# Optimization experiments

Hardware: AMD Instinct MI355X
Metric: run time of the kernel (lower is better)

## Reference

```python
import jax, jax.numpy as jnp
import numpy as np

B, C, T, H, W = 2, 512, 4, 32, 32
NH = 8          # num_heads
GROUPS = 32     # GroupNorm groups
EPS = 1e-5      # GroupNorm eps (torch default)


def setup_inputs() -> dict:
    key = jax.random.key(0)
    k0, k1, k2 = jax.random.split(key, 3)
    s = 0.02
    return {
        "x": jax.random.normal(k0, (B, C, T, H, W), jnp.float32),
        "gn_w": jnp.ones((C,), jnp.float32),
        "gn_b": jnp.zeros((C,), jnp.float32),
        "qkv_w": jax.random.normal(k1, (3 * C, C), jnp.float32) * s,
        "qkv_b": jnp.zeros((3 * C,), jnp.float32),
        "out_w": jax.random.normal(k2, (C, C), jnp.float32) * s,
        "out_b": jnp.zeros((C,), jnp.float32),
    }


def reference(x, gn_w, gn_b, qkv_w, qkv_b, out_w, out_b):
    Bb, Cc, Tt, Hh, Ww = x.shape
    N = Tt * Hh * Ww
    hd = Cc // NH

    # GroupNorm(32, C): normalize over (C//G, T, H, W) per group, biased var
    xg = x.reshape(Bb, GROUPS, -1)
    mean = jnp.mean(xg, axis=-1, keepdims=True)
    var = jnp.var(xg, axis=-1, keepdims=True)
    h = ((xg - mean) * jax.lax.rsqrt(var + EPS)).reshape(Bb, Cc, N)
    h = h * gn_w[None, :, None] + gn_b[None, :, None]

    # 1x1 Conv3d qkv == per-token linear over channels
    qkv = jnp.einsum('oc,bcn->bon', qkv_w, h) + qkv_b[None, :, None]
    qkv = qkv.reshape(Bb, 3, NH, hd, N).transpose(1, 0, 2, 4, 3)  # [3,B,nh,N,hd]
    q, k, v = qkv[0], qkv[1], qkv[2]

    scale = 1.0 / np.sqrt(hd).astype(np.float32)
    attn = jax.nn.softmax(jnp.einsum('bhnd,bhmd->bhnm', q, k) * scale, axis=-1)
    o = jnp.einsum('bhnm,bhmd->bhnd', attn, v)  # [B,nh,N,hd]

    # Faithful to original: h.permute(1,2,0,3).reshape(B,C,T,H,W)
    o = o.transpose(1, 2, 0, 3).reshape(Bb, Cc, N)
    o = jnp.einsum('oc,bcn->bon', out_w, o) + out_b[None, :, None]
    return x + o.reshape(Bb, Cc, Tt, Hh, Ww)
```

## Files before the change

### kernel.cpp

```cpp
#include <hip/hip_runtime.h>
#include <stdint.h>

#define B_    2
#define C_    512
#define NH_   8
#define HD_   64
#define N_    4096
#define G_    32
#define K_    512
#define EPS_  1e-5f
#define QSCALE_ 0.18033688011112042f

typedef __bf16 bf16;
typedef __attribute__((ext_vector_type(8))) __bf16 bf16x8;
typedef __attribute__((ext_vector_type(4))) float f32x4;

__global__ __launch_bounds__(256) void prep_k(const float* __restrict__ qkv_w,
                                              const float* __restrict__ out_w,
                                              const float* __restrict__ x,
                                              bf16* __restrict__ qkvwb,
                                              bf16* __restrict__ outwb,
                                              float* __restrict__ part) {
  const int blk = blockIdx.x;
  const int t = threadIdx.x;
  if (blk < 1024) {
    const int i = blk * 256 + t;
    const int n0 = (3 * C_ * C_) / 4;
    const float* s = (i < n0) ? qkv_w : out_w;
    bf16* d = (i < n0) ? qkvwb : outwb;
    const int k = (i < n0) ? i : i - n0;
    f32x4 v = *reinterpret_cast<const f32x4*>(s + (size_t)k * 4);
    bf16 o[4] = {(bf16)v[0], (bf16)v[1], (bf16)v[2], (bf16)v[3]};
    *reinterpret_cast<uint64_t*>(d + (size_t)k * 4) = *reinterpret_cast<uint64_t*>(o);
  } else {
    const int bb = blk - 1024;
    const float* p = x + (size_t)bb * 16384;
    float s1 = 0.f, s2 = 0.f;
    for (int i = 0; i < 16; ++i) {
      f32x4 v = *reinterpret_cast<const f32x4*>(p + (size_t)(i * 256 + t) * 4);
#pragma unroll
      for (int j = 0; j < 4; ++j) { float f = v[j]; s1 += f; s2 += f * f; }
    }
#pragma unroll
    for (int o = 32; o > 0; o >>= 1) { s1 += __shfl_down(s1, o); s2 += __shfl_down(s2, o); }
    __shared__ float a1[4], a2[4];
    if ((t & 63) == 0) { a1[t >> 6] = s1; a2[t >> 6] = s2; }
    __syncthreads();
    if (t == 0) {
      part[bb * 2]     = a1[0] + a1[1] + a1[2] + a1[3];
      part[bb * 2 + 1] = a2[0] + a2[1] + a2[2] + a2[3];
    }
  }
}

__global__ __launch_bounds__(256) void gn_apply_k(const float* __restrict__ x,
                                                  const float* __restrict__ part,
                                                  const float* __restrict__ gw,
                                                  const float* __restrict__ gb,
                                                  bf16* __restrict__ hT) {
  __shared__ float tile[64][65];
  const int n0 = blockIdx.x * 64, c0 = blockIdx.y * 64, b = blockIdx.z;
  const int t = threadIdx.x;
  {
    const int cc = t >> 2;
    const int nn = (t & 3) * 16;
    const int c = c0 + cc;
    const int bg = b * G_ + (c >> 4);
    float s1 = 0.f, s2 = 0.f;
#pragma unroll
    for (int q = 0; q < 4; ++q) {
      s1 += part[(bg * 4 + q) * 2];
      s2 += part[(bg * 4 + q) * 2 + 1];
    }
    const float mean = s1 * (1.f / 65536.f);
    const float var  = s2 * (1.f / 65536.f) - mean * mean;
    const float rstd = rsqrtf(var + EPS_);
    const float sw = gw[c] * rstd;
    const float sb = gb[c] - mean * sw;
    const float* xp = x + ((size_t)(b * C_ + c)) * N_ + n0 + nn;
#pragma unroll
    for (int q = 0; q < 4; ++q) {
      f32x4 v = *reinterpret_cast<const f32x4*>(xp + q * 4);
#pragma unroll
      for (int j = 0; j < 4; ++j) tile[cc][nn + q * 4 + j] = v[j] * sw + sb;
    }
  }
  __syncthreads();
  {
    const int rn = t >> 2;
    const int ch = (t & 3) * 16;
    bf16* hp = hT + ((size_t)b * N_ + n0 + rn) * C_ + c0 + ch;
    bf16x8 o0, o1;
#pragma unroll
    for (int j = 0; j < 8; ++j) {
      o0[j] = (bf16)tile[ch + j][rn];
      o1[j] = (bf16)tile[ch + 8 + j][rn];
    }
    *reinterpret_cast<bf16x8*>(hp)     = o0;
    *reinterpret_cast<bf16x8*>(hp + 8) = o1;
  }
}

template <int EPI>
__global__ __launch_bounds__(256) void gemm_bt_k(const bf16* __restrict__ A,
                                                 const bf16* __restrict__ BT,
                                                 const float* __restrict__ bias,
                                                 bf16* __restrict__ out0,
                                                 bf16* __restrict__ out1,
                                                 bf16* __restrict__ out2,
                                                 float* __restrict__ outf,
                                                 const float* __restrict__ xres) {
  __shared__ __align__(16) bf16 As[128][72];
  __shared__ __align__(16) bf16 Bs[128][72];
  const int t = threadIdx.x;
  const int w = t >> 6, lane = t & 63;
  const int quad = lane >> 4, l15 = lane & 15;
  const int m0 = blockIdx.y * 128, n0 = blockIdx.x * 128, b = blockIdx.z;
  const bf16* Ab = A + (size_t)m0 * K_;
  const bf16* Bb = BT + ((size_t)b * N_ + n0) * K_;
  const int srow = t >> 1;
  const int sk = (t & 1) * 32;

  f32x4 acc[4][4] = {};

  for (int kc = 0; kc < K_ / 64; ++kc) {
    __syncthreads();
    {
      const bf16* ag = Ab + (size_t)srow * K_ + kc * 64 + sk;
      const bf16* bg = Bb + (size_t)srow * K_ + kc * 64 + sk;
#pragma unroll
      for (int c = 0; c < 4; ++c) {
        *reinterpret_cast<bf16x8*>(&As[srow][sk + c * 8]) = *reinterpret_cast<const bf16x8*>(ag + c * 8);
        *reinterpret_cast<bf16x8*>(&Bs[srow][sk + c * 8]) = *reinterpret_cast<const bf16x8*>(bg + c * 8);
      }
    }
    __syncthreads();
    bf16x8 af[4][2], bfv[4][2];
#pragma unroll
    for (int i = 0; i < 4; ++i) {
      af[i][0] = *reinterpret_cast<const bf16x8*>(&As[(w >> 1) * 64 + i * 16 + l15][quad * 8]);
      af[i][1] = *reinterpret_cast<const bf16x8*>(&As[(w >> 1) * 64 + i * 16 + l15][quad * 8 + 32]);
    }
#pragma unroll
    for (int j = 0; j < 4; ++j) {
      bfv[j][0] = *reinterpret_cast<const bf16x8*>(&Bs[(w & 1) * 64 + j * 16 + l15][quad * 8]);
      bfv[j][1] = *reinterpret_cast<const bf16x8*>(&Bs[(w & 1) * 64 + j * 16 + l15][quad * 8 + 32]);
    }
#pragma unroll
    for (int i = 0; i < 4; ++i)
#pragma unroll
      for (int j = 0; j < 4; ++j) {
        acc[i][j] = __builtin_amdgcn_mfma_f32_16x16x32_bf16(af[i][0], bfv[j][0], acc[i][j], 0, 0, 0);
        acc[i][j] = __builtin_amdgcn_mfma_f32_16x16x32_bf16(af[i][1], bfv[j][1], acc[i][j], 0, 0, 0);
      }
  }

  const int rowbase = m0 + (w >> 1) * 64;
  const int colbase = n0 + (w & 1) * 64;
  if (EPI == 0) {
    const int which = m0 >> 9;
    if (which < 2) {
      bf16* dst = (which == 0) ? out0 : out1;
      const float sc = (which == 0) ? (float)QSCALE_ : 1.0f;
#pragma unroll
      for (int i = 0; i < 4; ++i) {
        const int mbase = rowbase + i * 16 + quad * 4;
        const int head = (mbase >> 6) & 7, d0 = mbase & 63;
        float bi[4];
#pragma unroll
        for (int r = 0; r < 4; ++r) bi[r] = bias[mbase + r];
#pragma unroll
        for (int j = 0; j < 4; ++j) {
          const int n = colbase + j * 16 + l15;
          union { bf16 h[4]; uint64_t u; } pk;
#pragma unroll
          for (int r = 0; r < 4; ++r) pk.h[r] = (bf16)((acc[i][j][r] + bi[r]) * sc);
          *reinterpret_cast<uint64_t*>(dst + ((size_t)(b * NH_ + head) * N_ + n) * HD_ + d0) = pk.u;
        }
      }
    } else {
#pragma unroll
      for (int i = 0; i < 4; ++i) {
        const int mbase = rowbase + i * 16 + quad * 4;
        const int head = (mbase >> 6) & 7;
#pragma unroll
        for (int r = 0; r < 4; ++r) {
          const int d = (mbase + r) & 63;
          const float bi = bias[mbase + r];
#pragma unroll
          for (int j = 0; j < 4; ++j) {
            const int n = colbase + j * 16 + l15;
            out2[((size_t)(b * NH_ + head) * HD_ + d) * N_ + n] = (bf16)(acc[i][j][r] + bi);
          }
        }
      }
    }
  } else {
#pragma unroll
    for (int i = 0; i < 4; ++i) {
#pragma unroll
      for (int r = 0; r < 4; ++r) {
        const int m = rowbase + i * 16 + quad * 4 + r;
        const float bi = bias[m];
#pragma unroll
        for (int j = 0; j < 4; ++j) {
          const int n = colbase + j * 16 + l15;
          const size_t idx = ((size_t)(b * C_ + m)) * N_ + n;
          outf[idx] = acc[i][j][r] + bi + xres[idx];
        }
      }
    }
  }
}

__global__ __launch_bounds__(512, 4) void attn_k(const bf16* __restrict__ qb,
                                                 const bf16* __restrict__ kb,
                                                 const bf16* __restrict__ vb,
                                                 bf16* __restrict__ oT) {
  __shared__ __align__(16) char smem[55296];
  bf16* Ps = (bf16*)(smem + 36864);
  bf16* Ot = (bf16*)smem;

  const int t = threadIdx.x;
  const int w = t >> 6, lane = t & 63, quad = lane >> 4, l15 = lane & 15;
  const int rblk = blockIdx.x;
  const int bh = blockIdx.y, head = bh & 7, b = bh >> 3;
  const bf16* qh = qb + (size_t)bh * N_ * HD_;
  const bf16* kh = kb + (size_t)bh * N_ * HD_;
  const bf16* vh = vb + (size_t)bh * HD_ * N_;

  bf16x8 qa0, qa1;
  {
    const bf16* qp = qh + ((size_t)((w * 16 + l15) * 32 + rblk)) * HD_ + quad * 8;
    qa0 = *reinterpret_cast<const bf16x8*>(qp);
    qa1 = *reinterpret_cast<const bf16x8*>(qp + 32);
  }

  f32x4 acc[4] = {};
  float lsum[4] = {};

  const int j = t >> 3;
  const int c8 = (t & 7) * 8;
  const int pj = (j & 3) * 16 + (j >> 2);
  bf16* Pw = Ps + w * 16 * 72;

  {
    bf16x8 kr = *reinterpret_cast<const bf16x8*>(kh + (size_t)j * HD_ + c8);
    bf16x8 vr = *reinterpret_cast<const bf16x8*>(vh + (size_t)j * N_ + c8);
    *reinterpret_cast<bf16x8*>((bf16*)smem + pj * 72 + c8) = kr;
    *reinterpret_cast<bf16x8*>((bf16*)(smem + 9216) + j * 72 + c8) = vr;
  }
  __syncthreads();

  for (int kt = 0; kt < 64; ++kt) {
    bf16* curK = (bf16*)(smem + (kt & 1) * 18432);
    bf16* curV = (bf16*)(smem + (kt & 1) * 18432 + 9216);

    bf16x8 kr, vr;
    if (kt != 63) {
      kr = *reinterpret_cast<const bf16x8*>(kh + ((size_t)(kt + 1) * 64 + j) * HD_ + c8);
      vr = *reinterpret_cast<const bf16x8*>(vh + (size_t)j * N_ + (kt + 1) * 64 + c8);
    }

    bf16x8 kf0[4], kf1[4];
#pragma unroll
    for (int mt = 0; mt < 4; ++mt) {
      kf0[mt] = *reinterpret_cast<const bf16x8*>(curK + (mt * 16 + l15) * 72 + quad * 8);
      kf1[mt] = *reinterpret_cast<const bf16x8*>(curK + (mt * 16 + l15) * 72 + quad * 8 + 32);
    }
    f32x4 S[4];
#pragma unroll
    for (int mt = 0; mt < 4; ++mt) {
      f32x4 zz = {0.f, 0.f, 0.f, 0.f};
      zz = __builtin_amdgcn_mfma_f32_16x16x32_bf16(qa0, kf0[mt], zz, 0, 0, 0);
      S[mt] = __builtin_amdgcn_mfma_f32_16x16x32_bf16(qa1, kf1[mt], zz, 0, 0, 0);
    }
#pragma unroll
    for (int r = 0; r < 4; ++r) {
      float p0 = __builtin_amdgcn_exp2f(S[0][r]);
      float p1 = __builtin_amdgcn_exp2f(S[1][r]);
      float p2 = __builtin_amdgcn_exp2f(S[2][r]);
      float p3 = __builtin_amdgcn_exp2f(S[3][r]);
      lsum[r] += (p0 + p1) + (p2 + p3);
      union { bf16 h[4]; uint64_t u; } pk;
      pk.h[0] = (bf16)p0; pk.h[1] = (bf16)p1; pk.h[2] = (bf16)p2; pk.h[3] = (bf16)p3;
      *reinterpret_cast<uint64_t*>(Pw + (quad * 4 + r) * 72 + l15 * 4) = pk.u;
    }
    asm volatile("s_waitcnt lgkmcnt(0)" ::: "memory");
    bf16x8 pa0 = *reinterpret_cast<const bf16x8*>(Pw + l15 * 72 + quad * 8);
    bf16x8 pa1 = *reinterpret_cast<const bf16x8*>(Pw + l15 * 72 + quad * 8 + 32);
#pragma unroll
    for (int dt = 0; dt < 4; ++dt) {
      bf16x8 vf0 = *reinterpret_cast<const bf16x8*>(curV + (dt * 16 + l15) * 72 + quad * 8);
      bf16x8 vf1 = *reinterpret_cast<const bf16x8*>(curV + (dt * 16 + l15) * 72 + quad * 8 + 32);
      acc[dt] = __builtin_amdgcn_mfma_f32_16x16x32_bf16(pa0, vf0, acc[dt], 0, 0, 0);
      acc[dt] = __builtin_amdgcn_mfma_f32_16x16x32_bf16(pa1, vf1, acc[dt], 0, 0, 0);
    }

    if (kt != 63) {
      bf16* nK = (bf16*)(smem + ((kt + 1) & 1) * 18432);
      bf16* nV = (bf16*)(smem + ((kt + 1) & 1) * 18432 + 9216);
      *reinterpret_cast<bf16x8*>(nK + pj * 72 + c8) = kr;
      *reinterpret_cast<bf16x8*>(nV + j * 72 + c8) = vr;
    }
    __syncthreads();
  }

  float inv[4];
#pragma unroll
  for (int r = 0; r < 4; ++r) {
    float l = lsum[r];
#pragma unroll
    for (int o = 1; o < 16; o <<= 1) l += __shfl_xor(l, o);
    inv[r] = 1.f / l;
  }

#pragma unroll
  for (int dt = 0; dt < 4; ++dt) {
    union { bf16 h[4]; uint64_t u; } o4;
#pragma unroll
    for (int r = 0; r < 4; ++r) o4.h[r] = (bf16)(acc[dt][r] * inv[r]);
    *reinterpret_cast<uint64_t*>(Ot + (dt * 16 + l15) * 136 + w * 16 + quad * 4) = o4.u;
  }
  __syncthreads();
  {
    const int d = t >> 3, ic = (t & 7) * 16;
    bf16* op = oT + (size_t)(head >> 2) * N_ * C_ +
               ((size_t)(rblk * 128 + b * 64 + d)) * C_ + (head & 3) * 128 + ic;
    *reinterpret_cast<bf16x8*>(op)     = *reinterpret_cast<const bf16x8*>(Ot + d * 136 + ic);
    *reinterpret_cast<bf16x8*>(op + 8) = *reinterpret_cast<const bf16x8*>(Ot + d * 136 + ic + 8);
  }
}

extern "C" void kernel_launch(void* const* d_in, const int* in_sizes, int n_in,
                              void* d_out, int out_size, void* d_ws, size_t ws_size,
                              hipStream_t stream) {
  const float* x     = (const float*)d_in[0];
  const float* gn_w  = (const float*)d_in[1];
  const float* gn_b  = (const float*)d_in[2];
  const float* qkv_w = (const float*)d_in[3];
  const float* qkv_b = (const float*)d_in[4];
  const float* out_w = (const float*)d_in[5];
  const float* out_b = (const float*)d_in[6];
  float* out = (float*)d_out;

  char* ws = (char*)d_ws;
  const size_t SZ = (size_t)B_ * C_ * N_ * sizeof(bf16);
  float* part  = (float*)ws;
  bf16* hT    = (bf16*)(ws + 4096);
  bf16* qbuf  = (bf16*)(ws + 4096 + SZ);
  bf16* kbuf  = (bf16*)(ws + 4096 + 2 * SZ);
  bf16* vbuf  = (bf16*)(ws + 4096 + 3 * SZ);
  bf16* oT    = (bf16*)(ws + 4096 + 4 * SZ);
  bf16* qkvwb = (bf16*)(ws + 4096 + 5 * SZ);
  bf16* outwb = qkvwb + (size_t)3 * C_ * C_;

  prep_k<<<dim3(1280), dim3(256), 0, stream>>>(qkv_w, out_w, x, qkvwb, outwb, part);
  gn_apply_k<<<dim3(N_ / 64, C_ / 64, B_), dim3(256), 0, stream>>>(x, part, gn_w, gn_b, hT);
  gemm_bt_k<0><<<dim3(N_ / 128, (3 * C_) / 128, B_), dim3(256), 0, stream>>>(
      qkvwb, hT, qkv_b, qbuf, kbuf, vbuf, nullptr, nullptr);
  attn_k<<<dim3(32, B_ * NH_), dim3(512), 0, stream>>>(qbuf, kbuf, vbuf, oT);
  gemm_bt_k<1><<<dim3(N_ / 128, C_ / 128, B_), dim3(256), 0, stream>>>(
      outwb, oT, out_b, nullptr, nullptr, nullptr, out, x);
}
```

Before: 224.1 us.

## Halve attention block threads, each wave handles two query row tiles

```diff
diff --git a/kernel.cpp b/kernel.cpp
--- a/kernel.cpp
+++ b/kernel.cpp
@@ -213,7 +213,7 @@
   }
 }
 
-__global__ __launch_bounds__(512, 4) void attn_k(const bf16* __restrict__ qb,
+__global__ __launch_bounds__(256, 2) void attn_k(const bf16* __restrict__ qb,
                                                  const bf16* __restrict__ kb,
                                                  const bf16* __restrict__ vb,
                                                  bf16* __restrict__ oT) {
@@ -229,26 +229,32 @@
   const bf16* kh = kb + (size_t)bh * N_ * HD_;
   const bf16* vh = vb + (size_t)bh * HD_ * N_;
 
-  bf16x8 qa0, qa1;
+  bf16x8 qa[2][2];
+#pragma unroll
+  for (int b2 = 0; b2 < 2; ++b2) {
+    const int bd = w + 4 * b2;
+    const bf16* qp = qh + ((size_t)((bd * 16 + l15) * 32 + rblk)) * HD_ + quad * 8;
+    qa[b2][0] = *reinterpret_cast<const bf16x8*>(qp);
+    qa[b2][1] = *reinterpret_cast<const bf16x8*>(qp + 32);
+  }
+
+  f32x4 acc[2][4] = {};
+  float lsum[2][4] = {};
+
+  const int sr = t >> 3, sc = (t & 7) * 8;
+  const int s0 = (sr & 3) * 16 + (sr >> 2);
+  const int s1 = ((sr + 32) & 3) * 16 + ((sr + 32) >> 2);
+
   {
-    const bf16* qp = qh + ((size_t)((w * 16 + l15) * 32 + rblk)) * HD_ + quad * 8;
-    qa0 = *reinterpret_cast<const bf16x8*>(qp);
-    qa1 = *reinterpret_cast<const bf16x8*>(qp + 32);
-  }
-
-  f32x4 acc[4] = {};
-  float lsum[4] = {};
-
-  const int j = t >> 3;
-  const int c8 = (t & 7) * 8;
-  const int pj = (j & 3) * 16 + (j >> 2);
-  bf16* Pw = Ps + w * 16 * 72;
-
-  {
-    bf16x8 kr = *reinterpret_cast<const bf16x8*>(kh + (size_t)j * HD_ + c8);
-    bf16x8 vr = *reinterpret_cast<const bf16x8*>(vh + (size_t)j * N_ + c8);
-    *reinterpret_cast<bf16x8*>((bf16*)smem + pj * 72 + c8) = kr;
-    *reinterpret_cast<bf16x8*>((bf16*)(smem + 9216) + j * 72 + c8) = vr;
+    *reinterpret_cast<bf16x8*>((bf16*)smem + s0 * 72 + sc) =
+        *reinterpret_cast<const bf16x8*>(kh + (size_t)sr * HD_ + sc);
+    *reinterpret_cast<bf16x8*>((bf16*)smem + s1 * 72 + sc) =
+        *reinterpret_cast<const bf16x8*>(kh + (size_t)(sr + 32) * HD_ + sc);
+    bf16* Vb0 = (bf16*)(smem + 9216);
+    *reinterpret_cast<bf16x8*>(Vb0 + sr * 72 + sc) =
+        *reinterpret_cast<const bf16x8*>(vh + (size_t)sr * N_ + sc);
+    *reinterpret_cast<bf16x8*>(Vb0 + (sr + 32) * 72 + sc) =
+        *reinterpret_cast<const bf16x8*>(vh + (size_t)(sr + 32) * N_ + sc);
   }
   __syncthreads();
 
@@ -256,10 +262,14 @@
     bf16* curK = (bf16*)(smem + (kt & 1) * 18432);
     bf16* curV = (bf16*)(smem + (kt & 1) * 18432 + 9216);
 
-    bf16x8 kr, vr;
+    bf16x8 kr0, kr1, vr0, vr1;
     if (kt != 63) {
-      kr = *reinterpret_cast<const bf16x8*>(kh + ((size_t)(kt + 1) * 64 + j) * HD_ + c8);
-      vr = *reinterpret_cast<const bf16x8*>(vh + (size_t)j * N_ + (kt + 1) * 64 + c8);
+      const bf16* kg = kh + ((size_t)(kt + 1) * 64) * HD_;
+      kr0 = *reinterpret_cast<const bf16x8*>(kg + (size_t)sr * HD_ + sc);
+      kr1 = *reinterpret_cast<const bf16x8*>(kg + (size_t)(sr + 32) * HD_ + sc);
+      const bf16* vg = vh + (size_t)(kt + 1) * 64;
+      vr0 = *reinterpret_cast<const bf16x8*>(vg + (size_t)sr * N_ + sc);
+      vr1 = *reinterpret_cast<const bf16x8*>(vg + (size_t)(sr + 32) * N_ + sc);
     }
 
     bf16x8 kf0[4], kf1[4];
@@ -268,67 +278,89 @@
       kf0[mt] = *reinterpret_cast<const bf16x8*>(curK + (mt * 16 + l15) * 72 + quad * 8);
       kf1[mt] = *reinterpret_cast<const bf16x8*>(curK + (mt * 16 + l15) * 72 + quad * 8 + 32);
     }
-    f32x4 S[4];
-#pragma unroll
-    for (int mt = 0; mt < 4; ++mt) {
-      f32x4 zz = {0.f, 0.f, 0.f, 0.f};
-      zz = __builtin_amdgcn_mfma_f32_16x16x32_bf16(qa0, kf0[mt], zz, 0, 0, 0);
-      S[mt] = __builtin_amdgcn_mfma_f32_16x16x32_bf16(qa1, kf1[mt], zz, 0, 0, 0);
-    }
-#pragma unroll
-    for (int r = 0; r < 4; ++r) {
-      float p0 = __builtin_amdgcn_exp2f(S[0][r]);
-      float p1 = __builtin_amdgcn_exp2f(S[1][r]);
-      float p2 = __builtin_amdgcn_exp2f(S[2][r]);
-      float p3 = __builtin_amdgcn_exp2f(S[3][r]);
-      lsum[r] += (p0 + p1) + (p2 + p3);
-      union { bf16 h[4]; uint64_t u; } pk;
-      pk.h[0] = (bf16)p0; pk.h[1] = (bf16)p1; pk.h[2] = (bf16)p2; pk.h[3] = (bf16)p3;
-      *reinterpret_cast<uint64_t*>(Pw + (quad * 4 + r) * 72 + l15 * 4) = pk.u;
+
+#pragma unroll
+    for (int b2 = 0; b2 < 2; ++b2) {
+      f32x4 S[4];
+#pragma unroll
+      for (int mt = 0; mt < 4; ++mt) {
+        f32x4 zz = {0.f, 0.f, 0.f, 0.f};
+        zz = __builtin_amdgcn_mfma_f32_16x16x32_bf16(qa[b2][0], kf0[mt], zz, 0, 0, 0);
+        S[mt] = __builtin_amdgcn_mfma_f32_16x16x32_bf16(qa[b2][1], kf1[mt], zz, 0, 0, 0);
+      }
+      bf16* Pw = Ps + ((w << 1) | b2) * 1152;
+#pragma unroll
+      for (int r = 0; r < 4; ++r) {
+        float p0 = __builtin_amdgcn_exp2f(S[0][r]);
+        float p1 = __builtin_amdgcn_exp2f(S[1][r]);
+        float p2 = __builtin_amdgcn_exp2f(S[2][r]);
+        float p3 = __builtin_amdgcn_exp2f(S[3][r]);
+        lsum[b2][r] += (p0 + p1) + (p2 + p3);
+        union { bf16 h[4]; uint64_t u; } pk;
+        pk.h[0] = (bf16)p0; pk.h[1] = (bf16)p1; pk.h[2] = (bf16)p2; pk.h[3] = (bf16)p3;
+        *reinterpret_cast<uint64_t*>(Pw + (quad * 4 + r) * 72 + l15 * 4) = pk.u;
+      }
     }
     asm volatile("s_waitcnt lgkmcnt(0)" ::: "memory");
-    bf16x8 pa0 = *reinterpret_cast<const bf16x8*>(Pw + l15 * 72 + quad * 8);
-    bf16x8 pa1 = *reinterpret_cast<const bf16x8*>(Pw + l15 * 72 + quad * 8 + 32);
+    bf16x8 pa[2][2];
+#pragma unroll
+    for (int b2 = 0; b2 < 2; ++b2) {
+      bf16* Pw = Ps + ((w << 1) | b2) * 1152;
+      pa[b2][0] = *reinterpret_cast<const bf16x8*>(Pw + l15 * 72 + quad * 8);
+      pa[b2][1] = *reinterpret_cast<const bf16x8*>(Pw + l15 * 72 + quad * 8 + 32);
+    }
 #pragma unroll
     for (int dt = 0; dt < 4; ++dt) {
       bf16x8 vf0 = *reinterpret_cast<const bf16x8*>(curV + (dt * 16 + l15) * 72 + quad * 8);
       bf16x8 vf1 = *reinterpret_cast<const bf16x8*>(curV + (dt * 16 + l15) * 72 + quad * 8 + 32);
-      acc[dt] = __builtin_amdgcn_mfma_f32_16x16x32_bf16(pa0, vf0, acc[dt], 0, 0, 0);
-      acc[dt] = __builtin_amdgcn_mfma_f32_16x16x32_bf16(pa1, vf1, acc[dt], 0, 0, 0);
+      acc[0][dt] = __builtin_amdgcn_mfma_f32_16x16x32_bf16(pa[0][0], vf0, acc[0][dt], 0, 0, 0);
+      acc[0][dt] = __builtin_amdgcn_mfma_f32_16x16x32_bf16(pa[0][1], vf1, acc[0][dt], 0, 0, 0);
+      acc[1][dt] = __builtin_amdgcn_mfma_f32_16x16x32_bf16(pa[1][0], vf0, acc[1][dt], 0, 0, 0);
+      acc[1][dt] = __builtin_amdgcn_mfma_f32_16x16x32_bf16(pa[1][1], vf1, acc[1][dt], 0, 0, 0);
     }
 
     if (kt != 63) {
       bf16* nK = (bf16*)(smem + ((kt + 1) & 1) * 18432);
       bf16* nV = (bf16*)(smem + ((kt + 1) & 1) * 18432 + 9216);
-      *reinterpret_cast<bf16x8*>(nK + pj * 72 + c8) = kr;
-      *reinterpret_cast<bf16x8*>(nV + j * 72 + c8) = vr;
+      *reinterpret_cast<bf16x8*>(nK + s0 * 72 + sc) = kr0;
+      *reinterpret_cast<bf16x8*>(nK + s1 * 72 + sc) = kr1;
+      *reinterpret_cast<bf16x8*>(nV + sr * 72 + sc) = vr0;
+      *reinterpret_cast<bf16x8*>(nV + (sr + 32) * 72 + sc) = vr1;
     }
     __syncthreads();
   }
 
-  float inv[4];
-#pragma unroll
-  for (int r = 0; r < 4; ++r) {
-    float l = lsum[r];
-#pragma unroll
-    for (int o = 1; o < 16; o <<= 1) l += __shfl_xor(l, o);
-    inv[r] = 1.f / l;
-  }
-
-#pragma unroll
-  for (int dt = 0; dt < 4; ++dt) {
-    union { bf16 h[4]; uint64_t u; } o4;
-#pragma unroll
-    for (int r = 0; r < 4; ++r) o4.h[r] = (bf16)(acc[dt][r] * inv[r]);
-    *reinterpret_cast<uint64_t*>(Ot + (dt * 16 + l15) * 136 + w * 16 + quad * 4) = o4.u;
+  float inv[2][4];
+#pragma unroll
+  for (int b2 = 0; b2 < 2; ++b2)
+#pragma unroll
+    for (int r = 0; r < 4; ++r) {
+      float l = lsum[b2][r];
+#pragma unroll
+      for (int o = 1; o < 16; o <<= 1) l += __shfl_xor(l, o);
+      inv[b2][r] = 1.f / l;
+    }
+
+#pragma unroll
+  for (int b2 = 0; b2 < 2; ++b2) {
+    const int bd = w + 4 * b2;
+#pragma unroll
+    for (int dt = 0; dt < 4; ++dt) {
+      union { bf16 h[4]; uint64_t u; } o4;
+#pragma unroll
+      for (int r = 0; r < 4; ++r) o4.h[r] = (bf16)(acc[b2][dt][r] * inv[b2][r]);
+      *reinterpret_cast<uint64_t*>(Ot + (dt * 16 + l15) * 136 + bd * 16 + quad * 4) = o4.u;
+    }
   }
   __syncthreads();
   {
-    const int d = t >> 3, ic = (t & 7) * 16;
+    const int d = t >> 2, ic = (t & 3) * 32;
     bf16* op = oT + (size_t)(head >> 2) * N_ * C_ +
                ((size_t)(rblk * 128 + b * 64 + d)) * C_ + (head & 3) * 128 + ic;
-    *reinterpret_cast<bf16x8*>(op)     = *reinterpret_cast<const bf16x8*>(Ot + d * 136 + ic);
-    *reinterpret_cast<bf16x8*>(op + 8) = *reinterpret_cast<const bf16x8*>(Ot + d * 136 + ic + 8);
+#pragma unroll
+    for (int c = 0; c < 4; ++c)
+      *reinterpret_cast<bf16x8*>(op + c * 8) =
+          *reinterpret_cast<const bf16x8*>(Ot + d * 136 + ic + c * 8);
   }
 }
 
@@ -359,7 +391,7 @@
   gn_apply_k<<<dim3(N_ / 64, C_ / 64, B_), dim3(256), 0, stream>>>(x, part, gn_w, gn_b, hT);
   gemm_bt_k<0><<<dim3(N_ / 128, (3 * C_) / 128, B_), dim3(256), 0, stream>>>(
       qkvwb, hT, qkv_b, qbuf, kbuf, vbuf, nullptr, nullptr);
-  attn_k<<<dim3(32, B_ * NH_), dim3(512), 0, stream>>>(qbuf, kbuf, vbuf, oT);
+  attn_k<<<dim3(32, B_ * NH_), dim3(256), 0, stream>>>(qbuf, kbuf, vbuf, oT);
   gemm_bt_k<1><<<dim3(N_ / 128, C_ / 128, B_), dim3(256), 0, stream>>>(
       outwb, oT, out_b, nullptr, nullptr, nullptr, out, x);
 }
```

After: 215.8 us. 1.04x faster.
